# Kernel tuning notes

Measured on AMD Instinct MI355X. Metric: run time of the kernel, lower is better.

Reference implementation:

```python
import jax, jax.numpy as jnp
import numpy as np

ND, NS = 50000, 30000
FD = FS = 256
H = 256
E = 1000000
EL = 200000


def _lin_init(key, fan_in, fan_out):
    # torch Linear default: U(-1/sqrt(fan_in), 1/sqrt(fan_in)) for W and b
    kw, kb = jax.random.split(key)
    bound = 1.0 / np.sqrt(fan_in)
    W = jax.random.uniform(kw, (fan_in, fan_out), jnp.float32, -bound, bound)
    b = jax.random.uniform(kb, (fan_out,), jnp.float32, -bound, bound)
    return W, b


def setup_inputs() -> dict:
    key = jax.random.key(0)
    ks = jax.random.split(key, 16)
    x_drug = jax.random.normal(ks[0], (ND, FD), jnp.float32)
    x_disease = jax.random.normal(ks[1], (NS, FS), jnp.float32)
    edge_src = jax.random.randint(ks[2], (E,), 0, ND, jnp.int64)
    edge_dst = jax.random.randint(ks[3], (E,), 0, NS, jnp.int64)
    label_row = jax.random.randint(ks[4], (EL,), 0, ND, jnp.int64)
    label_col = jax.random.randint(ks[5], (EL,), 0, NS, jnp.int64)
    # SAGEConv params per layer per edge type: lin_l (on aggregated src, with bias),
    # lin_r (on dst root, no bias). Edge types: ds = drug->disease, sd = disease->drug (rev).
    Wl1_ds, bl1_ds = _lin_init(ks[6], FD, H)
    Wr1_ds, _ = _lin_init(ks[7], FS, H)
    Wl1_sd, bl1_sd = _lin_init(ks[8], FS, H)
    Wr1_sd, _ = _lin_init(ks[9], FD, H)
    Wl2_ds, bl2_ds = _lin_init(ks[10], H, H)
    Wr2_ds, _ = _lin_init(ks[11], H, H)
    Wl2_sd, bl2_sd = _lin_init(ks[12], H, H)
    Wr2_sd, _ = _lin_init(ks[13], H, H)
    Wdec1, bdec1 = _lin_init(ks[14], 2 * H, H)
    Wdec2, bdec2 = _lin_init(ks[15], H, 1)
    return dict(x_drug=x_drug, x_disease=x_disease,
                edge_src=edge_src, edge_dst=edge_dst,
                label_row=label_row, label_col=label_col,
                Wl1_ds=Wl1_ds, bl1_ds=bl1_ds, Wr1_ds=Wr1_ds,
                Wl1_sd=Wl1_sd, bl1_sd=bl1_sd, Wr1_sd=Wr1_sd,
                Wl2_ds=Wl2_ds, bl2_ds=bl2_ds, Wr2_ds=Wr2_ds,
                Wl2_sd=Wl2_sd, bl2_sd=bl2_sd, Wr2_sd=Wr2_sd,
                Wdec1=Wdec1, bdec1=bdec1, Wdec2=Wdec2, bdec2=bdec2)


def _mean_agg(x_src, src, dst, n_dst):
    # gather source features per edge, mean-scatter into destinations
    msg = x_src[src]                                         # [E, F]
    s = jax.ops.segment_sum(msg, dst, num_segments=n_dst)    # [n_dst, F]
    cnt = jax.ops.segment_sum(jnp.ones_like(dst, x_src.dtype), dst, num_segments=n_dst)
    return s / jnp.maximum(cnt, 1.0)[:, None]


def _sage_layer(x_drug, x_dis, src, dst,
                Wl_ds, bl_ds, Wr_ds, Wl_sd, bl_sd, Wr_sd):
    z_dis = _mean_agg(x_drug, src, dst, NS) @ Wl_ds + bl_ds + x_dis @ Wr_ds
    z_drug = _mean_agg(x_dis, dst, src, ND) @ Wl_sd + bl_sd + x_drug @ Wr_sd
    return z_drug, z_dis


def reference(x_drug, x_disease, edge_src, edge_dst, label_row, label_col,
              Wl1_ds, bl1_ds, Wr1_ds, Wl1_sd, bl1_sd, Wr1_sd,
              Wl2_ds, bl2_ds, Wr2_ds, Wl2_sd, bl2_sd, Wr2_sd,
              Wdec1, bdec1, Wdec2, bdec2):
    # layer 1 (relu)
    zd, zs = _sage_layer(x_drug, x_disease, edge_src, edge_dst,
                         Wl1_ds, bl1_ds, Wr1_ds, Wl1_sd, bl1_sd, Wr1_sd)
    zd, zs = jax.nn.relu(zd), jax.nn.relu(zs)
    # layer 2 (no relu, last layer)
    zd, zs = _sage_layer(zd, zs, edge_src, edge_dst,
                         Wl2_ds, bl2_ds, Wr2_ds, Wl2_sd, bl2_sd, Wr2_sd)
    # edge decoder
    z = jnp.concatenate([zd[label_row], zs[label_col]], axis=-1)  # [EL, 2H]
    h = jax.nn.relu(z @ Wdec1 + bdec1)
    out = (h @ Wdec2 + bdec2).reshape(-1)
    return out
```

## Files before the change

kernel.cpp:

```cpp
#include <hip/hip_runtime.h>
#include <hip/hip_bf16.h>

#define ND 50000
#define NS 30000
#define NE 1000000
#define EL 200000
#define NTOT (NS + ND)
#define SCAN_BLK ((NTOT + 1023) / 1024)

#define ZERO_BLKS ((NTOT + 255) / 256)
#define TRW4_BLKS 1024
#define COMP_BLKS 64
#define BIAS_BLKS 2
#define WPREP_BLKS (ZERO_BLKS + TRW4_BLKS + COMP_BLKS + BIAS_BLKS)

#define RANK_BLKS ((NE + 255) / 256)
#define NB_D (391 * 2)
#define NB_S (235 * 2)
#define GEMM1_BLKS (2 * NB_D + 2 * NB_S)
#define MEGA_GRP 1252
#define MEGA_BLKS (RANK_BLKS + GEMM1_BLKS)

typedef short short8 __attribute__((ext_vector_type(8)));
typedef float f32x4 __attribute__((ext_vector_type(4)));

__device__ __forceinline__ float b2f(unsigned short u) {
    union { unsigned int i; float f; } c; c.i = ((unsigned int)u) << 16; return c.f;
}
__device__ __forceinline__ unsigned short f2b(float f) {
    __hip_bfloat16 h = __float2bfloat16(f);
    union { __hip_bfloat16 h; unsigned short u; } c; c.h = h; return c.u;
}

__device__ __forceinline__ void gload_lds16(const unsigned short* g, unsigned short* l) {
    __builtin_amdgcn_global_load_lds(
        (const __attribute__((address_space(1))) unsigned int*)g,
        (__attribute__((address_space(3))) unsigned int*)l, 16, 0, 0);
}

struct WAll {
    const float* w1[4];
    const float* w2[4];
    const float* wdec1;
    const float* bl2_ds;
    const float* bl2_sd;
};


__global__ __launch_bounds__(256) void wprep(int* __restrict__ cnt, WAll wa,
                                             unsigned short* __restrict__ Wt,
                                             float* __restrict__ cbuf) {
    int b = blockIdx.x, t = threadIdx.x;
    if (b < ZERO_BLKS) {
        int i = b * 256 + t;
        if (i < NTOT) cnt[i] = 0;
    } else if (b < ZERO_BLKS + TRW4_BLKS) {
        int o = (b - ZERO_BLKS) * 256 + t;
        int mat = o >> 16, i2 = o & 65535;
        int n = i2 >> 8, k = i2 & 255;
        Wt[o] = f2b(wa.w1[mat][k * 256 + n]);
    } else if (b < ZERO_BLKS + TRW4_BLKS + COMP_BLKS) {
        int idx = b - ZERO_BLKS - TRW4_BLKS;
        int mat = idx >> 4;
        int k0 = (idx & 15) * 16;
        const float* W2 = wa.w2[mat];
        const float* Wd = wa.wdec1 + ((mat < 2) ? 65536 : 0);
        float acc[16] = {};
        const int n = t;
        for (int j = 0; j < 256; ++j) {
            float wd = Wd[j * 256 + n];
#pragma unroll
            for (int k = 0; k < 16; ++k) acc[k] += W2[(k0 + k) * 256 + j] * wd;
        }
        unsigned short* dst = Wt + (size_t)(4 + mat) * 65536 + n * 256 + k0;
#pragma unroll
        for (int k = 0; k < 16; ++k) dst[k] = f2b(acc[k]);
    } else {
        int idx = b - ZERO_BLKS - TRW4_BLKS - COMP_BLKS;
        const float* bsrc = idx ? wa.bl2_sd : wa.bl2_ds;
        const float* Wd = wa.wdec1 + (idx ? 0 : 65536);
        float acc = 0.f;
        const int n = t;
        for (int j = 0; j < 256; ++j) acc += bsrc[j] * Wd[j * 256 + n];
        cbuf[idx * 256 + n] = acc;
    }
}

__global__ __launch_bounds__(256) void mega(const int* __restrict__ esrc,
                                            const int* __restrict__ edst,
                                            int* cnt_drug, int* cnt_dis,
                                            unsigned short* __restrict__ rank_sd,
                                            unsigned short* __restrict__ rank_ds,
                                            const float* __restrict__ xd,
                                            const float* __restrict__ xs,
                                            const unsigned short* __restrict__ Wt,
                                            unsigned short* __restrict__ PA0,
                                            unsigned short* __restrict__ RA3,
                                            unsigned short* __restrict__ PB2,
                                            unsigned short* __restrict__ RB1) {
    __shared__ unsigned short As[128 * 64];
    __shared__ unsigned short Bs[128 * 64];
    const int b = blockIdx.x, t = threadIdx.x;
    int role, idx;
    if (b < 5 * MEGA_GRP) {
        int g = b / 5, r = b - g * 5;
        if (r < 3) { role = 0; idx = g * 3 + r; }
        else       { role = 1; idx = g * 2 + r - 3; }
    } else {
        role = 0; idx = 3 * MEGA_GRP + (b - 5 * MEGA_GRP);
    }

    if (role == 0) {
        int i = idx * 256 + t;
        if (i < NE) {
            int s = esrc[i], d = edst[i];
            rank_ds[i] = (unsigned short)atomicAdd(&cnt_dis[d], 1);
            rank_sd[i] = (unsigned short)atomicAdd(&cnt_drug[s], 1);
        }
        return;
    }

    int gi = idx;
    const float* Xf; const unsigned short* Bt; unsigned short* C; int M;
    if (gi < NB_D)            { Xf = xd; Bt = Wt + 0 * 65536; C = PA0; M = ND; }
    else if (gi < 2 * NB_D)   { gi -= NB_D;            Xf = xd; Bt = Wt + 3 * 65536; C = RA3; M = ND; }
    else if (gi < 2 * NB_D + NB_S) { gi -= 2 * NB_D;   Xf = xs; Bt = Wt + 2 * 65536; C = PB2; M = NS; }
    else                      { gi -= 2 * NB_D + NB_S; Xf = xs; Bt = Wt + 1 * 65536; C = RB1; M = NS; }
    const int bm0 = (gi >> 1) * 128;
    const int n0b = (gi & 1) * 128;

    const int lane = t & 63, w = t >> 6;
    const int wr = w >> 1, wc = w & 1;
    const int fr = lane & 15, g = lane >> 4;
    const int r8 = lane >> 3, slotL = lane & 7;
    const int ar_ = t >> 1, ah = t & 1;
    int ra = bm0 + ar_; if (ra >= M) ra = M - 1;
    const int arm = ar_ & 7;

    f32x4 acc[4][4];
#pragma unroll
    for (int m = 0; m < 4; ++m)
#pragma unroll
        for (int n = 0; n < 4; ++n)
            acc[m][n] = (f32x4){0.f, 0.f, 0.f, 0.f};

    for (int st = 0; st < 4; ++st) {
        const int k0 = st * 64;
#pragma unroll
        for (int j = 0; j < 4; ++j) {
            const int is = w * 4 + j;
            const int rowb = is * 8 + r8;
            const int sl = slotL ^ (rowb & 7);
            gload_lds16(Bt + (size_t)(n0b + rowb) * 256 + k0 + sl * 8, &Bs[is * 512]);
        }
        {
            const float* arow = Xf + (size_t)ra * 256 + k0 + ah * 32;
            unsigned short* awr = &As[ar_ * 64];
#pragma unroll
            for (int q2 = 0; q2 < 4; ++q2) {
                const int q = ah * 4 + q2;
                float4 f0 = *reinterpret_cast<const float4*>(arow + q2 * 8);
                float4 f1 = *reinterpret_cast<const float4*>(arow + q2 * 8 + 4);
                short8 v;
                v[0] = (short)f2b(f0.x); v[1] = (short)f2b(f0.y);
                v[2] = (short)f2b(f0.z); v[3] = (short)f2b(f0.w);
                v[4] = (short)f2b(f1.x); v[5] = (short)f2b(f1.y);
                v[6] = (short)f2b(f1.z); v[7] = (short)f2b(f1.w);
                *reinterpret_cast<short8*>(awr + (q ^ arm) * 8) = v;
            }
        }
        __syncthreads();
#pragma unroll
        for (int kc = 0; kc < 2; ++kc) {
            const int q = kc * 4 + g;
            short8 a[4], bb[4];
#pragma unroll
            for (int n = 0; n < 4; ++n) {
                const int br = wc * 64 + n * 16 + fr;
                bb[n] = *reinterpret_cast<const short8*>(&Bs[br * 64 + (q ^ (fr & 7)) * 8]);
            }
#pragma unroll
            for (int m = 0; m < 4; ++m) {
                const int arr = wr * 64 + m * 16 + fr;
                a[m] = *reinterpret_cast<const short8*>(&As[arr * 64 + (q ^ (fr & 7)) * 8]);
            }
#pragma unroll
            for (int m = 0; m < 4; ++m)
#pragma unroll
                for (int n = 0; n < 4; ++n)
                    acc[m][n] = __builtin_amdgcn_mfma_f32_16x16x32_bf16(a[m], bb[n], acc[m][n], 0, 0, 0);
        }
        __syncthreads();
    }

#pragma unroll
    for (int n = 0; n < 4; ++n) {
        const int col = n0b + wc * 64 + n * 16 + fr;
#pragma unroll
        for (int m = 0; m < 4; ++m) {
#pragma unroll
            for (int r = 0; r < 4; ++r) {
                int row = bm0 + wr * 64 + m * 16 + g * 4 + r;
                if (row < M) C[row * 256 + col] = f2b(acc[m][n][r]);
            }
        }
    }
}


__global__ __launch_bounds__(256) void scan_part(const int* __restrict__ cnt,
                                                 int* __restrict__ bsum) {
    __shared__ int red[4];
    int t = threadIdx.x, lane = t & 63, wid = t >> 6;
    int base = blockIdx.x * 1024 + t * 4;
    int s = 0;
    if (base < NTOT) {
        int4 c = *reinterpret_cast<const int4*>(cnt + base);
        s = c.x + c.y + c.z + c.w;
    }
#pragma unroll
    for (int off = 32; off; off >>= 1) s += __shfl_down(s, off);
    if (lane == 0) red[wid] = s;
    __syncthreads();
    if (t == 0) bsum[blockIdx.x] = red[0] + red[1] + red[2] + red[3];
}

__global__ void scan_top(int* bsum, int nb) {
    int lane = threadIdx.x;
    int a0 = lane < nb ? bsum[lane] : 0;
    int a1 = (64 + lane) < nb ? bsum[64 + lane] : 0;
    int i0 = a0, i1 = a1;
#pragma unroll
    for (int off = 1; off < 64; off <<= 1) {
        int t0 = __shfl_up(i0, off);
        int t1 = __shfl_up(i1, off);
        if (lane >= off) { i0 += t0; i1 += t1; }
    }
    int tot0 = __shfl(i0, 63);
    if (lane < nb) bsum[lane] = i0 - a0;
    if (64 + lane < nb) bsum[64 + lane] = tot0 + i1 - a1;
}

__global__ __launch_bounds__(256) void scan_emit(const int* __restrict__ cnt,
                                                 const int* __restrict__ boff,
                                                 int* __restrict__ row_dis,
                                                 int* __restrict__ row_drug,
                                                 float* __restrict__ inv_dis,
                                                 float* __restrict__ inv_drug) {
    __shared__ int wsum[4];
    int t = threadIdx.x, lane = t & 63, wid = t >> 6;
    int base = blockIdx.x * 1024 + t * 4;
    int4 c = make_int4(0, 0, 0, 0);
    if (base < NTOT) c = *reinterpret_cast<const int4*>(cnt + base);
    int sl = c.x + c.y + c.z + c.w;
    int sc = sl;
#pragma unroll
    for (int off = 1; off < 64; off <<= 1) {
        int tv = __shfl_up(sc, off);
        if (lane >= off) sc += tv;
    }
    if (lane == 63) wsum[wid] = sc;
    __syncthreads();
    int woff = 0;
    for (int w2 = 0; w2 < wid; ++w2) woff += wsum[w2];
    int run = boff[blockIdx.x] + woff + (sc - sl);
    int cc[4] = { c.x, c.y, c.z, c.w };
    if (base < NTOT) {
#pragma unroll
        for (int k = 0; k < 4; ++k) {
            int i = base + k;
            float iv = 1.0f / (float)(cc[k] > 1 ? cc[k] : 1);
            if (i < NS) { row_dis[i] = run; inv_dis[i] = iv; }
            else        { row_drug[i - NS] = run - NE; inv_drug[i - NS] = iv; }
            run += cc[k];
        }
    }
    if (blockIdx.x == 0 && t == 0) { row_dis[NS] = NE; row_drug[ND] = NE; }
}

__global__ void place_kernel(const int* __restrict__ src, const int* __restrict__ dst,
                             const int* __restrict__ row_drug, const int* __restrict__ row_dis,
                             const unsigned short* __restrict__ rank_sd,
                             const unsigned short* __restrict__ rank_ds,
                             unsigned short* __restrict__ val_sd,
                             unsigned short* __restrict__ val_ds, int n) {
    int i = blockIdx.x * blockDim.x + threadIdx.x;
    if (i < n) {
        int s = src[i], d = dst[i];
        val_ds[row_dis[d] + (int)rank_ds[i]] = (unsigned short)s;
        val_sd[row_drug[s] + (int)rank_sd[i]] = (unsigned short)d;
    }
}


__global__ __launch_bounds__(256) void agg_fused(const unsigned short* __restrict__ gatherDrug,
                                                 const unsigned short* __restrict__ gatherDis,
                                                 const int* __restrict__ row_dis,
                                                 const int* __restrict__ row_drug,
                                                 const unsigned short* __restrict__ val_ds,
                                                 const unsigned short* __restrict__ val_sd,
                                                 const float* __restrict__ inv_dis,
                                                 const float* __restrict__ inv_drug,
                                                 const unsigned short* __restrict__ dirDis,
                                                 const unsigned short* __restrict__ dirDrug,
                                                 const float* __restrict__ bDis,
                                                 const float* __restrict__ bDrug,
                                                 unsigned short* __restrict__ outDis,
                                                 unsigned short* __restrict__ outDrug,
                                                 int do_relu) {
    int wid = threadIdx.x >> 6, lane = threadIdx.x & 63;
    int node = blockIdx.x * 4 + wid;
    const int half = lane >> 5;
    const int sub = lane & 31;
    const unsigned short* xsrc; const int* row; const unsigned short* vals;
    const float* inv; const unsigned short* dirp; const float* bias; unsigned short* outp;
    if (node < NS) {
        xsrc = gatherDrug; row = row_dis; vals = val_ds; inv = inv_dis;
        dirp = dirDis; bias = bDis; outp = outDis;
    } else {
        node -= NS;
        if (node >= ND) return;
        xsrc = gatherDis; row = row_drug; vals = val_sd; inv = inv_drug;
        dirp = dirDrug; bias = bDrug; outp = outDrug;
    }
    const int beg = row[node], end = row[node + 1];
    const int off = sub * 8;
    float a[8] = {};
    int j = beg;
    for (; j + 8 <= end; j += 8) {
        int r0 = vals[j     + half];
        int r1 = vals[j + 2 + half];
        int r2 = vals[j + 4 + half];
        int r3 = vals[j + 6 + half];
        short8 v0 = *reinterpret_cast<const short8*>(xsrc + r0 * 256 + off);
        short8 v1 = *reinterpret_cast<const short8*>(xsrc + r1 * 256 + off);
        short8 v2 = *reinterpret_cast<const short8*>(xsrc + r2 * 256 + off);
        short8 v3 = *reinterpret_cast<const short8*>(xsrc + r3 * 256 + off);
#pragma unroll
        for (int k = 0; k < 8; ++k)
            a[k] += b2f((unsigned short)v0[k]) + b2f((unsigned short)v1[k])
                  + b2f((unsigned short)v2[k]) + b2f((unsigned short)v3[k]);
    }
    for (; j + 2 <= end; j += 2) {
        int r = vals[j + half];
        short8 v = *reinterpret_cast<const short8*>(xsrc + r * 256 + off);
#pragma unroll
        for (int k = 0; k < 8; ++k) a[k] += b2f((unsigned short)v[k]);
    }
    if (j < end && half == 0) {
        int r = vals[j];
        short8 v = *reinterpret_cast<const short8*>(xsrc + r * 256 + off);
#pragma unroll
        for (int k = 0; k < 8; ++k) a[k] += b2f((unsigned short)v[k]);
    }
#pragma unroll
    for (int k = 0; k < 8; ++k) a[k] += __shfl_xor(a[k], 32);
    if (half == 0) {
        const float iv = inv[node];
        short8 dir = *reinterpret_cast<const short8*>(dirp + node * 256 + off);
        float4 b0 = *reinterpret_cast<const float4*>(bias + off);
        float4 b1 = *reinterpret_cast<const float4*>(bias + off + 4);
        float bb[8] = { b0.x, b0.y, b0.z, b0.w, b1.x, b1.y, b1.z, b1.w };
        short8 o;
#pragma unroll
        for (int k = 0; k < 8; ++k) {
            float v = a[k] * iv + b2f((unsigned short)dir[k]) + bb[k];
            if (do_relu) v = fmaxf(v, 0.f);
            o[k] = (short)f2b(v);
        }
        *reinterpret_cast<short8*>(outp + node * 256 + off) = o;
    }
}


struct Seg1 {
    const unsigned short* A;
    const unsigned short* Bt;
    unsigned short* C;
    int M; int nblk;
};

__global__ __launch_bounds__(256) void gemm_lds4(Seg1 s0, Seg1 s1, Seg1 s2, Seg1 s3) {
    __shared__ unsigned short As[128 * 64];
    __shared__ unsigned short Bs[128 * 64];
    Seg1 s;
    int bx = blockIdx.x;
    if (bx < s0.nblk) s = s0;
    else if (bx < s0.nblk + s1.nblk) { s = s1; bx -= s0.nblk; }
    else if (bx < s0.nblk + s1.nblk + s2.nblk) { s = s2; bx -= s0.nblk + s1.nblk; }
    else { s = s3; bx -= s0.nblk + s1.nblk + s2.nblk; }

    const int t = threadIdx.x;
    const int lane = t & 63, w = t >> 6;
    const int wr = w >> 1, wc = w & 1;
    const int fr = lane & 15, g = lane >> 4;
    const int bm0 = bx * 128;
    const int n0b = (int)blockIdx.y * 128;
    const int M = s.M;
    const int r8 = lane >> 3, slotL = lane & 7;

    f32x4 acc[4][4];
#pragma unroll
    for (int m = 0; m < 4; ++m)
#pragma unroll
        for (int n = 0; n < 4; ++n)
            acc[m][n] = (f32x4){0.f, 0.f, 0.f, 0.f};

    for (int st = 0; st < 4; ++st) {
        const int k0 = st * 64;
#pragma unroll
        for (int j = 0; j < 4; ++j) {
            const int is = w * 4 + j;
            const int row = is * 8 + r8;
            const int sl = slotL ^ (row & 7);
            int ra = bm0 + row; if (ra >= M) ra = M - 1;
            gload_lds16(s.A + (size_t)ra * 256 + k0 + sl * 8, &As[is * 512]);
            gload_lds16(s.Bt + (size_t)(n0b + row) * 256 + k0 + sl * 8, &Bs[is * 512]);
        }
        __syncthreads();
#pragma unroll
        for (int kc = 0; kc < 2; ++kc) {
            const int q = kc * 4 + g;
            short8 a[4], b[4];
#pragma unroll
            for (int n = 0; n < 4; ++n) {
                const int br = wc * 64 + n * 16 + fr;
                b[n] = *reinterpret_cast<const short8*>(&Bs[br * 64 + (q ^ (fr & 7)) * 8]);
            }
#pragma unroll
            for (int m = 0; m < 4; ++m) {
                const int ar = wr * 64 + m * 16 + fr;
                a[m] = *reinterpret_cast<const short8*>(&As[ar * 64 + (q ^ (fr & 7)) * 8]);
            }
#pragma unroll
            for (int m = 0; m < 4; ++m)
#pragma unroll
                for (int n = 0; n < 4; ++n)
                    acc[m][n] = __builtin_amdgcn_mfma_f32_16x16x32_bf16(a[m], b[n], acc[m][n], 0, 0, 0);
        }
        __syncthreads();
    }

#pragma unroll
    for (int n = 0; n < 4; ++n) {
        const int col = n0b + wc * 64 + n * 16 + fr;
#pragma unroll
        for (int m = 0; m < 4; ++m) {
#pragma unroll
            for (int r = 0; r < 4; ++r) {
                int row = bm0 + wr * 64 + m * 16 + g * 4 + r;
                if (row < M) s.C[row * 256 + col] = f2b(acc[m][n][r]);
            }
        }
    }
}


__global__ __launch_bounds__(256) void dec_edge(const unsigned short* __restrict__ Pd,
                                                const unsigned short* __restrict__ Ps,
                                                const int* __restrict__ lrow,
                                                const int* __restrict__ lcol,
                                                const float* __restrict__ b1,
                                                const float* __restrict__ w2,
                                                const float* __restrict__ b2,
                                                float* __restrict__ outp, int n) {
    int wid = threadIdx.x >> 6, lane = threadIdx.x & 63;
    int half = lane >> 5, sl = lane & 31;
    int e = blockIdx.x * 8 + wid * 2 + half;
    if (e >= n) return;
    int r = lrow[e], c = lcol[e];
    const int off = sl * 8;
    short8 pd = *reinterpret_cast<const short8*>(Pd + r * 256 + off);
    short8 ps = *reinterpret_cast<const short8*>(Ps + c * 256 + off);
    float s = 0.f;
#pragma unroll
    for (int k = 0; k < 8; ++k) {
        float h = b2f((unsigned short)pd[k]) + b2f((unsigned short)ps[k]) + b1[off + k];
        s += fmaxf(h, 0.f) * w2[off + k];
    }
#pragma unroll
    for (int o = 16; o; o >>= 1) s += __shfl_down(s, o, 32);
    if (sl == 0) outp[e] = s + b2[0];
}


extern "C" void kernel_launch(void* const* d_in, const int* in_sizes, int n_in,
                              void* d_out, int out_size, void* d_ws, size_t ws_size,
                              hipStream_t stream) {
    const float* x_drug = (const float*)d_in[0];
    const float* x_dis  = (const float*)d_in[1];
    const int* esrc = (const int*)d_in[2];
    const int* edst = (const int*)d_in[3];
    const int* lrow = (const int*)d_in[4];
    const int* lcol = (const int*)d_in[5];
    const float* Wl1_ds = (const float*)d_in[6];
    const float* bl1_ds = (const float*)d_in[7];
    const float* Wr1_ds = (const float*)d_in[8];
    const float* Wl1_sd = (const float*)d_in[9];
    const float* bl1_sd = (const float*)d_in[10];
    const float* Wr1_sd = (const float*)d_in[11];
    const float* Wl2_ds = (const float*)d_in[12];
    const float* bl2_ds = (const float*)d_in[13];
    const float* Wr2_ds = (const float*)d_in[14];
    const float* Wl2_sd = (const float*)d_in[15];
    const float* bl2_sd = (const float*)d_in[16];
    const float* Wr2_sd = (const float*)d_in[17];
    const float* Wdec1 = (const float*)d_in[18];
    const float* bdec1 = (const float*)d_in[19];
    const float* Wdec2 = (const float*)d_in[20];
    const float* bdec2 = (const float*)d_in[21];
    float* outp = (float*)d_out;

    char* ws = (char*)d_ws;
    size_t off = 0;
    auto alloc = [&](size_t bytes) -> void* {
        void* p = ws + off;
        off = (off + bytes + 255) & ~(size_t)255;
        return p;
    };
    int* cnt       = (int*)alloc((size_t)NTOT * 4);
    int* bsum      = (int*)alloc((size_t)SCAN_BLK * 4);
    int* row_dis   = (int*)alloc((size_t)(NS + 1) * 4);
    int* row_drug  = (int*)alloc((size_t)(ND + 1) * 4);
    float* inv_dis = (float*)alloc((size_t)NS * 4);
    float* inv_drug= (float*)alloc((size_t)ND * 4);
    float* cbuf    = (float*)alloc((size_t)512 * 4);
    unsigned short* rank_ds = (unsigned short*)alloc((size_t)NE * 2);
    unsigned short* rank_sd = (unsigned short*)alloc((size_t)NE * 2);
    unsigned short* val_ds  = (unsigned short*)alloc((size_t)NE * 2);
    unsigned short* val_sd  = (unsigned short*)alloc((size_t)NE * 2);
    unsigned short* Wt   = (unsigned short*)alloc((size_t)8 * 65536 * 2);
    unsigned short* PA0  = (unsigned short*)alloc((size_t)ND * 256 * 2);
    unsigned short* RA3  = (unsigned short*)alloc((size_t)ND * 256 * 2);
    unsigned short* PB2  = (unsigned short*)alloc((size_t)NS * 256 * 2);
    unsigned short* RB1  = (unsigned short*)alloc((size_t)NS * 256 * 2);
    unsigned short* zs1  = (unsigned short*)alloc((size_t)NS * 256 * 2);
    unsigned short* zd1  = (unsigned short*)alloc((size_t)ND * 256 * 2);
    unsigned short* Ps   = (unsigned short*)alloc((size_t)NS * 256 * 2);
    unsigned short* Pd   = (unsigned short*)alloc((size_t)ND * 256 * 2);
    int* cnt_dis = cnt;
    int* cnt_drug = cnt + NS;

    WAll wa;
    wa.w1[0] = Wl1_ds; wa.w1[1] = Wr1_ds; wa.w1[2] = Wl1_sd; wa.w1[3] = Wr1_sd;
    wa.w2[0] = Wl2_ds; wa.w2[1] = Wr2_ds; wa.w2[2] = Wl2_sd; wa.w2[3] = Wr2_sd;
    wa.wdec1 = Wdec1; wa.bl2_ds = bl2_ds; wa.bl2_sd = bl2_sd;
    wprep<<<WPREP_BLKS, 256, 0, stream>>>(cnt, wa, Wt, cbuf);

    mega<<<MEGA_BLKS, 256, 0, stream>>>(esrc, edst, cnt_drug, cnt_dis, rank_sd, rank_ds,
                                        x_drug, x_dis, Wt, PA0, RA3, PB2, RB1);

    scan_part<<<SCAN_BLK, 256, 0, stream>>>(cnt, bsum);
    scan_top<<<1, 64, 0, stream>>>(bsum, SCAN_BLK);
    scan_emit<<<SCAN_BLK, 256, 0, stream>>>(cnt, bsum, row_dis, row_drug, inv_dis, inv_drug);
    place_kernel<<<(NE + 255) / 256, 256, 0, stream>>>(esrc, edst, row_drug, row_dis,
                                                       rank_sd, rank_ds, val_sd, val_ds, NE);

    const int AGG_GRID = (NTOT + 3) / 4;

    agg_fused<<<AGG_GRID, 256, 0, stream>>>(PA0, PB2, row_dis, row_drug, val_ds, val_sd,
                                            inv_dis, inv_drug, RB1, RA3, bl1_ds, bl1_sd,
                                            zs1, zd1, 1);

    unsigned short* G1 = PA0;
    unsigned short* G4 = RA3;
    unsigned short* G2 = PB2;
    unsigned short* G3 = RB1;
    {
        Seg1 a = { zd1, Wt + (size_t)4 * 65536, G1, ND, 391 };
        Seg1 b = { zs1, Wt + (size_t)5 * 65536, G2, NS, 235 };
        Seg1 c = { zs1, Wt + (size_t)6 * 65536, G3, NS, 235 };
        Seg1 d = { zd1, Wt + (size_t)7 * 65536, G4, ND, 391 };
        dim3 grid(391 + 235 + 235 + 391, 2);
        gemm_lds4<<<grid, 256, 0, stream>>>(a, b, c, d);
    }

    agg_fused<<<AGG_GRID, 256, 0, stream>>>(G1, G3, row_dis, row_drug, val_ds, val_sd,
                                            inv_dis, inv_drug, G2, G4, cbuf, cbuf + 256,
                                            Ps, Pd, 0);

    dec_edge<<<(EL + 7) / 8, 256, 0, stream>>>(Pd, Ps, lrow, lcol, bdec1, Wdec2, bdec2, outp, EL);
}
```

Measured before the change: 527.8 us.

## Regroup kernels: co-schedule edge ranking with weight prep, and placement with GEMM

The edge-rank atomics are moved out of the GEMM kernel and interleaved with the weight transpose and precompute work in one launch. The CSR placement scatter is merged into the layer-1 GEMM kernel with interleaved block roles. Counter zeroing moves to a memset. The aim is to overlap latency-bound atomic and scatter work with compute-bound work in different phases and to drop one launch. The GEMM now waits for the scan chain, so it no longer overlaps the ranking atomics.

```diff
diff --git a/kernel.cpp b/kernel.cpp
--- a/kernel.cpp
+++ b/kernel.cpp
@@ -8,18 +8,19 @@
 #define NTOT (NS + ND)
 #define SCAN_BLK ((NTOT + 1023) / 1024)
 
-#define ZERO_BLKS ((NTOT + 255) / 256)
+#define RANK_BLKS ((NE + 255) / 256)
 #define TRW4_BLKS 1024
 #define COMP_BLKS 64
 #define BIAS_BLKS 2
-#define WPREP_BLKS (ZERO_BLKS + TRW4_BLKS + COMP_BLKS + BIAS_BLKS)
-
-#define RANK_BLKS ((NE + 255) / 256)
+#define WROLE_BLKS (TRW4_BLKS + COMP_BLKS + BIAS_BLKS)
+#define RW_GRP 977
+#define RW_BLKS (5 * RW_GRP + (WROLE_BLKS - RW_GRP))
+
 #define NB_D (391 * 2)
 #define NB_S (235 * 2)
 #define GEMM1_BLKS (2 * NB_D + 2 * NB_S)
-#define MEGA_GRP 1252
-#define MEGA_BLKS (RANK_BLKS + GEMM1_BLKS)
+#define PG_GRP 1252
+#define PG_BLKS (5 * PG_GRP + (RANK_BLKS - 3 * PG_GRP))
 
 typedef short short8 __attribute__((ext_vector_type(8)));
 typedef float f32x4 __attribute__((ext_vector_type(4)));
@@ -46,23 +47,42 @@
     const float* bl2_sd;
 };
 
-
-__global__ __launch_bounds__(256) void wprep(int* __restrict__ cnt, WAll wa,
-                                             unsigned short* __restrict__ Wt,
-                                             float* __restrict__ cbuf) {
-    int b = blockIdx.x, t = threadIdx.x;
-    if (b < ZERO_BLKS) {
-        int i = b * 256 + t;
-        if (i < NTOT) cnt[i] = 0;
-    } else if (b < ZERO_BLKS + TRW4_BLKS) {
-        int o = (b - ZERO_BLKS) * 256 + t;
+__global__ __launch_bounds__(256) void rank_w(const int* __restrict__ esrc,
+                                              const int* __restrict__ edst,
+                                              int* cnt_drug, int* cnt_dis,
+                                              unsigned short* __restrict__ rank_sd,
+                                              unsigned short* __restrict__ rank_ds,
+                                              WAll wa,
+                                              unsigned short* __restrict__ Wt,
+                                              float* __restrict__ cbuf) {
+    const int b = blockIdx.x, t = threadIdx.x;
+    int role, idx;
+    if (b < 5 * RW_GRP) {
+        int g = b / 5, r = b - g * 5;
+        if (r < 4) { role = 0; idx = g * 4 + r; }
+        else       { role = 1; idx = g; }
+    } else {
+        role = 1; idx = RW_GRP + (b - 5 * RW_GRP);
+    }
+
+    if (role == 0) {
+        int i = idx * 256 + t;
+        if (i < NE) {
+            int s = esrc[i], d = edst[i];
+            rank_ds[i] = (unsigned short)atomicAdd(&cnt_dis[d], 1);
+            rank_sd[i] = (unsigned short)atomicAdd(&cnt_drug[s], 1);
+        }
+        return;
+    }
+    if (idx < TRW4_BLKS) {
+        int o = idx * 256 + t;
         int mat = o >> 16, i2 = o & 65535;
         int n = i2 >> 8, k = i2 & 255;
         Wt[o] = f2b(wa.w1[mat][k * 256 + n]);
-    } else if (b < ZERO_BLKS + TRW4_BLKS + COMP_BLKS) {
-        int idx = b - ZERO_BLKS - TRW4_BLKS;
-        int mat = idx >> 4;
-        int k0 = (idx & 15) * 16;
+    } else if (idx < TRW4_BLKS + COMP_BLKS) {
+        int ci = idx - TRW4_BLKS;
+        int mat = ci >> 4;
+        int k0 = (ci & 15) * 16;
         const float* W2 = wa.w2[mat];
         const float* Wd = wa.wdec1 + ((mat < 2) ? 65536 : 0);
         float acc[16] = {};
@@ -76,134 +96,13 @@
 #pragma unroll
         for (int k = 0; k < 16; ++k) dst[k] = f2b(acc[k]);
     } else {
-        int idx = b - ZERO_BLKS - TRW4_BLKS - COMP_BLKS;
-        const float* bsrc = idx ? wa.bl2_sd : wa.bl2_ds;
-        const float* Wd = wa.wdec1 + (idx ? 0 : 65536);
+        int bi = idx - TRW4_BLKS - COMP_BLKS;
+        const float* bsrc = bi ? wa.bl2_sd : wa.bl2_ds;
+        const float* Wd = wa.wdec1 + (bi ? 0 : 65536);
         float acc = 0.f;
         const int n = t;
         for (int j = 0; j < 256; ++j) acc += bsrc[j] * Wd[j * 256 + n];
-        cbuf[idx * 256 + n] = acc;
-    }
-}
-
-__global__ __launch_bounds__(256) void mega(const int* __restrict__ esrc,
-                                            const int* __restrict__ edst,
-                                            int* cnt_drug, int* cnt_dis,
-                                            unsigned short* __restrict__ rank_sd,
-                                            unsigned short* __restrict__ rank_ds,
-                                            const float* __restrict__ xd,
-                                            const float* __restrict__ xs,
-                                            const unsigned short* __restrict__ Wt,
-                                            unsigned short* __restrict__ PA0,
-                                            unsigned short* __restrict__ RA3,
-                                            unsigned short* __restrict__ PB2,
-                                            unsigned short* __restrict__ RB1) {
-    __shared__ unsigned short As[128 * 64];
-    __shared__ unsigned short Bs[128 * 64];
-    const int b = blockIdx.x, t = threadIdx.x;
-    int role, idx;
-    if (b < 5 * MEGA_GRP) {
-        int g = b / 5, r = b - g * 5;
-        if (r < 3) { role = 0; idx = g * 3 + r; }
-        else       { role = 1; idx = g * 2 + r - 3; }
-    } else {
-        role = 0; idx = 3 * MEGA_GRP + (b - 5 * MEGA_GRP);
-    }
-
-    if (role == 0) {
-        int i = idx * 256 + t;
-        if (i < NE) {
-            int s = esrc[i], d = edst[i];
-            rank_ds[i] = (unsigned short)atomicAdd(&cnt_dis[d], 1);
-            rank_sd[i] = (unsigned short)atomicAdd(&cnt_drug[s], 1);
-        }
-        return;
-    }
-
-    int gi = idx;
-    const float* Xf; const unsigned short* Bt; unsigned short* C; int M;
-    if (gi < NB_D)            { Xf = xd; Bt = Wt + 0 * 65536; C = PA0; M = ND; }
-    else if (gi < 2 * NB_D)   { gi -= NB_D;            Xf = xd; Bt = Wt + 3 * 65536; C = RA3; M = ND; }
-    else if (gi < 2 * NB_D + NB_S) { gi -= 2 * NB_D;   Xf = xs; Bt = Wt + 2 * 65536; C = PB2; M = NS; }
-    else                      { gi -= 2 * NB_D + NB_S; Xf = xs; Bt = Wt + 1 * 65536; C = RB1; M = NS; }
-    const int bm0 = (gi >> 1) * 128;
-    const int n0b = (gi & 1) * 128;
-
-    const int lane = t & 63, w = t >> 6;
-    const int wr = w >> 1, wc = w & 1;
-    const int fr = lane & 15, g = lane >> 4;
-    const int r8 = lane >> 3, slotL = lane & 7;
-    const int ar_ = t >> 1, ah = t & 1;
-    int ra = bm0 + ar_; if (ra >= M) ra = M - 1;
-    const int arm = ar_ & 7;
-
-    f32x4 acc[4][4];
-#pragma unroll
-    for (int m = 0; m < 4; ++m)
-#pragma unroll
-        for (int n = 0; n < 4; ++n)
-            acc[m][n] = (f32x4){0.f, 0.f, 0.f, 0.f};
-
-    for (int st = 0; st < 4; ++st) {
-        const int k0 = st * 64;
-#pragma unroll
-        for (int j = 0; j < 4; ++j) {
-            const int is = w * 4 + j;
-            const int rowb = is * 8 + r8;
-            const int sl = slotL ^ (rowb & 7);
-            gload_lds16(Bt + (size_t)(n0b + rowb) * 256 + k0 + sl * 8, &Bs[is * 512]);
-        }
-        {
-            const float* arow = Xf + (size_t)ra * 256 + k0 + ah * 32;
-            unsigned short* awr = &As[ar_ * 64];
-#pragma unroll
-            for (int q2 = 0; q2 < 4; ++q2) {
-                const int q = ah * 4 + q2;
-                float4 f0 = *reinterpret_cast<const float4*>(arow + q2 * 8);
-                float4 f1 = *reinterpret_cast<const float4*>(arow + q2 * 8 + 4);
-                short8 v;
-                v[0] = (short)f2b(f0.x); v[1] = (short)f2b(f0.y);
-                v[2] = (short)f2b(f0.z); v[3] = (short)f2b(f0.w);
-                v[4] = (short)f2b(f1.x); v[5] = (short)f2b(f1.y);
-                v[6] = (short)f2b(f1.z); v[7] = (short)f2b(f1.w);
-                *reinterpret_cast<short8*>(awr + (q ^ arm) * 8) = v;
-            }
-        }
-        __syncthreads();
-#pragma unroll
-        for (int kc = 0; kc < 2; ++kc) {
-            const int q = kc * 4 + g;
-            short8 a[4], bb[4];
-#pragma unroll
-            for (int n = 0; n < 4; ++n) {
-                const int br = wc * 64 + n * 16 + fr;
-                bb[n] = *reinterpret_cast<const short8*>(&Bs[br * 64 + (q ^ (fr & 7)) * 8]);
-            }
-#pragma unroll
-            for (int m = 0; m < 4; ++m) {
-                const int arr = wr * 64 + m * 16 + fr;
-                a[m] = *reinterpret_cast<const short8*>(&As[arr * 64 + (q ^ (fr & 7)) * 8]);
-            }
-#pragma unroll
-            for (int m = 0; m < 4; ++m)
-#pragma unroll
-                for (int n = 0; n < 4; ++n)
-                    acc[m][n] = __builtin_amdgcn_mfma_f32_16x16x32_bf16(a[m], bb[n], acc[m][n], 0, 0, 0);
-        }
-        __syncthreads();
-    }
-
-#pragma unroll
-    for (int n = 0; n < 4; ++n) {
-        const int col = n0b + wc * 64 + n * 16 + fr;
-#pragma unroll
-        for (int m = 0; m < 4; ++m) {
-#pragma unroll
-            for (int r = 0; r < 4; ++r) {
-                int row = bm0 + wr * 64 + m * 16 + g * 4 + r;
-                if (row < M) C[row * 256 + col] = f2b(acc[m][n][r]);
-            }
-        }
+        cbuf[bi * 256 + n] = acc;
     }
 }
 
@@ -278,17 +177,127 @@
     if (blockIdx.x == 0 && t == 0) { row_dis[NS] = NE; row_drug[ND] = NE; }
 }
 
-__global__ void place_kernel(const int* __restrict__ src, const int* __restrict__ dst,
-                             const int* __restrict__ row_drug, const int* __restrict__ row_dis,
-                             const unsigned short* __restrict__ rank_sd,
-                             const unsigned short* __restrict__ rank_ds,
-                             unsigned short* __restrict__ val_sd,
-                             unsigned short* __restrict__ val_ds, int n) {
-    int i = blockIdx.x * blockDim.x + threadIdx.x;
-    if (i < n) {
-        int s = src[i], d = dst[i];
-        val_ds[row_dis[d] + (int)rank_ds[i]] = (unsigned short)s;
-        val_sd[row_drug[s] + (int)rank_sd[i]] = (unsigned short)d;
+__global__ __launch_bounds__(256) void place_gemm(const int* __restrict__ esrc,
+                                                  const int* __restrict__ edst,
+                                                  const int* __restrict__ row_drug,
+                                                  const int* __restrict__ row_dis,
+                                                  const unsigned short* __restrict__ rank_sd,
+                                                  const unsigned short* __restrict__ rank_ds,
+                                                  unsigned short* __restrict__ val_sd,
+                                                  unsigned short* __restrict__ val_ds,
+                                                  const float* __restrict__ xd,
+                                                  const float* __restrict__ xs,
+                                                  const unsigned short* __restrict__ Wt,
+                                                  unsigned short* __restrict__ PA0,
+                                                  unsigned short* __restrict__ RA3,
+                                                  unsigned short* __restrict__ PB2,
+                                                  unsigned short* __restrict__ RB1) {
+    __shared__ unsigned short As[128 * 64];
+    __shared__ unsigned short Bs[128 * 64];
+    const int b = blockIdx.x, t = threadIdx.x;
+    int role, idx;
+    if (b < 5 * PG_GRP) {
+        int g = b / 5, r = b - g * 5;
+        if (r < 3) { role = 0; idx = g * 3 + r; }
+        else       { role = 1; idx = g * 2 + r - 3; }
+    } else {
+        role = 0; idx = 3 * PG_GRP + (b - 5 * PG_GRP);
+    }
+
+    if (role == 0) {
+        int i = idx * 256 + t;
+        if (i < NE) {
+            int s = esrc[i], d = edst[i];
+            val_ds[row_dis[d] + (int)rank_ds[i]] = (unsigned short)s;
+            val_sd[row_drug[s] + (int)rank_sd[i]] = (unsigned short)d;
+        }
+        return;
+    }
+
+    int gi = idx;
+    const float* Xf; const unsigned short* Bt; unsigned short* C; int M;
+    if (gi < NB_D)            { Xf = xd; Bt = Wt + 0 * 65536; C = PA0; M = ND; }
+    else if (gi < 2 * NB_D)   { gi -= NB_D;            Xf = xd; Bt = Wt + 3 * 65536; C = RA3; M = ND; }
+    else if (gi < 2 * NB_D + NB_S) { gi -= 2 * NB_D;   Xf = xs; Bt = Wt + 2 * 65536; C = PB2; M = NS; }
+    else                      { gi -= 2 * NB_D + NB_S; Xf = xs; Bt = Wt + 1 * 65536; C = RB1; M = NS; }
+    const int bm0 = (gi >> 1) * 128;
+    const int n0b = (gi & 1) * 128;
+
+    const int lane = t & 63, w = t >> 6;
+    const int wr = w >> 1, wc = w & 1;
+    const int fr = lane & 15, g = lane >> 4;
+    const int r8 = lane >> 3, slotL = lane & 7;
+    const int ar_ = t >> 1, ah = t & 1;
+    int ra = bm0 + ar_; if (ra >= M) ra = M - 1;
+    const int arm = ar_ & 7;
+
+    f32x4 acc[4][4];
+#pragma unroll
+    for (int m = 0; m < 4; ++m)
+#pragma unroll
+        for (int n = 0; n < 4; ++n)
+            acc[m][n] = (f32x4){0.f, 0.f, 0.f, 0.f};
+
+    for (int st = 0; st < 4; ++st) {
+        const int k0 = st * 64;
+#pragma unroll
+        for (int j = 0; j < 4; ++j) {
+            const int is = w * 4 + j;
+            const int rowb = is * 8 + r8;
+            const int sl = slotL ^ (rowb & 7);
+            gload_lds16(Bt + (size_t)(n0b + rowb) * 256 + k0 + sl * 8, &Bs[is * 512]);
+        }
+        {
+            const float* arow = Xf + (size_t)ra * 256 + k0 + ah * 32;
+            unsigned short* awr = &As[ar_ * 64];
+#pragma unroll
+            for (int q2 = 0; q2 < 4; ++q2) {
+                const int q = ah * 4 + q2;
+                float4 f0 = *reinterpret_cast<const float4*>(arow + q2 * 8);
+                float4 f1 = *reinterpret_cast<const float4*>(arow + q2 * 8 + 4);
+                short8 v;
+                v[0] = (short)f2b(f0.x); v[1] = (short)f2b(f0.y);
+                v[2] = (short)f2b(f0.z); v[3] = (short)f2b(f0.w);
+                v[4] = (short)f2b(f1.x); v[5] = (short)f2b(f1.y);
+                v[6] = (short)f2b(f1.z); v[7] = (short)f2b(f1.w);
+                *reinterpret_cast<short8*>(awr + (q ^ arm) * 8) = v;
+            }
+        }
+        __syncthreads();
+#pragma unroll
+        for (int kc = 0; kc < 2; ++kc) {
+            const int q = kc * 4 + g;
+            short8 a[4], bb[4];
+#pragma unroll
+            for (int n = 0; n < 4; ++n) {
+                const int br = wc * 64 + n * 16 + fr;
+                bb[n] = *reinterpret_cast<const short8*>(&Bs[br * 64 + (q ^ (fr & 7)) * 8]);
+            }
+#pragma unroll
+            for (int m = 0; m < 4; ++m) {
+                const int arr = wr * 64 + m * 16 + fr;
+                a[m] = *reinterpret_cast<const short8*>(&As[arr * 64 + (q ^ (fr & 7)) * 8]);
+            }
+#pragma unroll
+            for (int m = 0; m < 4; ++m)
+#pragma unroll
+                for (int n = 0; n < 4; ++n)
+                    acc[m][n] = __builtin_amdgcn_mfma_f32_16x16x32_bf16(a[m], bb[n], acc[m][n], 0, 0, 0);
+        }
+        __syncthreads();
+    }
+
+#pragma unroll
+    for (int n = 0; n < 4; ++n) {
+        const int col = n0b + wc * 64 + n * 16 + fr;
+#pragma unroll
+        for (int m = 0; m < 4; ++m) {
+#pragma unroll
+            for (int r = 0; r < 4; ++r) {
+                int row = bm0 + wr * 64 + m * 16 + g * 4 + r;
+                if (row < M) C[row * 256 + col] = f2b(acc[m][n][r]);
+            }
+        }
     }
 }
 
@@ -541,20 +550,22 @@
     int* cnt_dis = cnt;
     int* cnt_drug = cnt + NS;
 
+    hipMemsetAsync(cnt, 0, (size_t)NTOT * 4, stream);
+
     WAll wa;
     wa.w1[0] = Wl1_ds; wa.w1[1] = Wr1_ds; wa.w1[2] = Wl1_sd; wa.w1[3] = Wr1_sd;
     wa.w2[0] = Wl2_ds; wa.w2[1] = Wr2_ds; wa.w2[2] = Wl2_sd; wa.w2[3] = Wr2_sd;
     wa.wdec1 = Wdec1; wa.bl2_ds = bl2_ds; wa.bl2_sd = bl2_sd;
-    wprep<<<WPREP_BLKS, 256, 0, stream>>>(cnt, wa, Wt, cbuf);
-
-    mega<<<MEGA_BLKS, 256, 0, stream>>>(esrc, edst, cnt_drug, cnt_dis, rank_sd, rank_ds,
-                                        x_drug, x_dis, Wt, PA0, RA3, PB2, RB1);
+    rank_w<<<RW_BLKS, 256, 0, stream>>>(esrc, edst, cnt_drug, cnt_dis,
+                                        rank_sd, rank_ds, wa, Wt, cbuf);
 
     scan_part<<<SCAN_BLK, 256, 0, stream>>>(cnt, bsum);
     scan_top<<<1, 64, 0, stream>>>(bsum, SCAN_BLK);
     scan_emit<<<SCAN_BLK, 256, 0, stream>>>(cnt, bsum, row_dis, row_drug, inv_dis, inv_drug);
-    place_kernel<<<(NE + 255) / 256, 256, 0, stream>>>(esrc, edst, row_drug, row_dis,
-                                                       rank_sd, rank_ds, val_sd, val_ds, NE);
+
+    place_gemm<<<PG_BLKS, 256, 0, stream>>>(esrc, edst, row_drug, row_dis,
+                                            rank_sd, rank_ds, val_sd, val_ds,
+                                            x_drug, x_dis, Wt, PA0, RA3, PB2, RB1);
 
     const int AGG_GRID = (NTOT + 3) / 4;
 
```

Result: slower. 576.1 us (+9.2%).
